# Optimization experiments

Measured on AMD Instinct MI355X. Metric: run time of the kernel, lower is better.

Reference implementation:

```python
import jax, jax.numpy as jnp
import numpy as np

EMBED_DIM = 768
NUM_HEADS = 12
HEAD_DIM = EMBED_DIM // NUM_HEADS


def setup_inputs() -> dict:
    key = jax.random.key(0)
    k_x, k_wqkv, k_bqkv, k_wp, k_bp = jax.random.split(key, 5)
    B, N, C = 4, 2048, EMBED_DIM
    # torch nn.Linear init scale ~ 1/sqrt(fan_in); use small normal for numerics
    s = 1.0 / np.sqrt(C)
    return {
        "x": jax.random.normal(k_x, (B, N, C), dtype=jnp.float32),
        "w_qkv": jax.random.normal(k_wqkv, (3 * C, C), dtype=jnp.float32) * s,  # torch [out,in]
        "b_qkv": jax.random.normal(k_bqkv, (3 * C,), dtype=jnp.float32) * s,
        "w_proj": jax.random.normal(k_wp, (C, C), dtype=jnp.float32) * s,
        "b_proj": jax.random.normal(k_bp, (C,), dtype=jnp.float32) * s,
    }


def reference(x, w_qkv, b_qkv, w_proj, b_proj):
    B, N, C = x.shape
    H, D = NUM_HEADS, HEAD_DIM
    scale = 1.0 / np.sqrt(D)
    # qkv linear: x @ W.T + b  -> [B,N,3C]
    qkv = jnp.einsum("bnc,oc->bno", x, w_qkv) + b_qkv
    qkv = qkv.reshape(B, N, 3, H, D).transpose(2, 0, 3, 1, 4)  # [3,B,H,N,D]
    q, k, v = qkv[0], qkv[1], qkv[2]
    attn = jnp.einsum("bhnd,bhmd->bhnm", q, k) * scale  # [B,H,N,N]
    attn = jax.nn.softmax(attn, axis=-1)
    out = jnp.einsum("bhnm,bhmd->bhnd", attn, v)  # [B,H,N,D]
    out = out.transpose(0, 2, 1, 3).reshape(B, N, C)
    return jnp.einsum("bnc,oc->bno", out, w_proj) + b_proj
```

## Files before the change

### kernel.cpp

```cpp
#include <hip/hip_runtime.h>
#include <hip/hip_bf16.h>
#include <math.h>

#define EMBED 768
#define NHEAD 12
#define HDIM 64
#define SEQ 2048
#define BATCH 4

typedef __hip_bfloat16 bf16;
typedef __attribute__((ext_vector_type(8))) short bf16x8;
typedef __attribute__((ext_vector_type(4))) short s16x4;
typedef __attribute__((ext_vector_type(4))) float f32x4;
typedef __attribute__((ext_vector_type(2))) unsigned int u32x2;

__device__ inline float b2f(bf16 v) { return __bfloat162float(v); }
__device__ inline bf16 f2b(float v) { return __float2bfloat16(v); }
__device__ inline unsigned pk2(float a, float b) {
  return (unsigned)__bfloat16_as_ushort(f2b(a)) |
         ((unsigned)__bfloat16_as_ushort(f2b(b)) << 16);
}

__device__ inline void gl_lds16(const bf16* g, bf16* l) {
  __builtin_amdgcn_global_load_lds(
      (const __attribute__((address_space(1))) void*)g,
      (__attribute__((address_space(3))) void*)l, 16, 0, 0);
}

#define NX4  (BATCH * SEQ * EMBED / 4)
#define NWQ4 (3 * EMBED * EMBED / 4)
#define NWP4 (EMBED * EMBED / 4)

__global__ __launch_bounds__(256) void cvt_all(
    const float* __restrict__ x, const float* __restrict__ wq,
    const float* __restrict__ wp, bf16* __restrict__ xb,
    bf16* __restrict__ wqb, bf16* __restrict__ wpb) {
  int i = blockIdx.x * 256 + threadIdx.x;
  const float* src;
  bf16* dst;
  int k;
  if (i < NX4) {
    src = x; dst = xb; k = i;
  } else if (i < NX4 + NWQ4) {
    src = wq; dst = wqb; k = i - NX4;
  } else if (i < NX4 + NWQ4 + NWP4) {
    src = wp; dst = wpb; k = i - NX4 - NWQ4;
  } else {
    return;
  }
  float4 v = ((const float4*)src)[k];
  s16x4 o;
  o[0] = (short)__bfloat16_as_ushort(f2b(v.x));
  o[1] = (short)__bfloat16_as_ushort(f2b(v.y));
  o[2] = (short)__bfloat16_as_ushort(f2b(v.z));
  o[3] = (short)__bfloat16_as_ushort(f2b(v.w));
  *(s16x4*)(dst + 4 * (size_t)k) = o;
}

template <int MODE, int TM>
__global__ __launch_bounds__(256, 4) void gemm_mfma(
    const bf16* __restrict__ A, const bf16* __restrict__ W,
    const float* __restrict__ bias, float* __restrict__ outF,
    bf16* __restrict__ outQ, bf16* __restrict__ outK, bf16* __restrict__ outV,
    int M, int N, int K) {
  __shared__ bf16 As[TM][64];
  __shared__ bf16 Bs[128][64];
  const int t = threadIdx.x;
  const int w = t >> 6;
  const int lane = t & 63;
  const int g = lane >> 4, c = lane & 15;
  const int m0 = blockIdx.y * TM, n0 = blockIdx.x * 128;
  constexpr int MJ = TM / 32;
  const int wr = (w >> 1) * (TM / 2);
  const int wc = (w & 1) * 64;

  const int srow = lane >> 3;
  const int l8 = lane & 7;
  const int sseg = (l8 ^ srow) * 8;

  f32x4 acc[4][MJ] = {};

  for (int k0 = 0; k0 < K; k0 += 64) {
#pragma unroll
    for (int i = 0; i < 4; i++) {
      int r = w * 32 + i * 8;
      gl_lds16(W + (size_t)(n0 + r + srow) * K + k0 + sseg, &Bs[r][0]);
    }
#pragma unroll
    for (int i = 0; i < TM / 32; i++) {
      int r = w * (TM / 4) + i * 8;
      gl_lds16(A + (size_t)(m0 + r + srow) * K + k0 + sseg, &As[r][0]);
    }
    __syncthreads();

#pragma unroll
    for (int h = 0; h < 2; h++) {
      bf16x8 xf[MJ], wf[4];
#pragma unroll
      for (int j = 0; j < MJ; j++)
        xf[j] = *(const bf16x8*)&As[wr + j * 16 + c][((h * 4 + g) ^ (c & 7)) * 8];
#pragma unroll
      for (int i = 0; i < 4; i++)
        wf[i] = *(const bf16x8*)&Bs[wc + i * 16 + c][((h * 4 + g) ^ (c & 7)) * 8];
#pragma unroll
      for (int i = 0; i < 4; i++)
#pragma unroll
        for (int j = 0; j < MJ; j++)
          acc[i][j] = __builtin_amdgcn_mfma_f32_16x16x32_bf16(wf[i], xf[j],
                                                              acc[i][j], 0, 0, 0);
    }
    __syncthreads();
  }

#pragma unroll
  for (int i = 0; i < 4; i++) {
    const int ob = n0 + wc + i * 16 + g * 4;
    const f32x4 bv = *(const f32x4*)&bias[ob];
    int which = 0, hh = 0, d0 = 0;
    if (MODE == 0) {
      which = ob / EMBED;
      int rem = ob - which * EMBED;
      hh = rem >> 6;
      d0 = rem & 63;
    }
#pragma unroll
    for (int j = 0; j < MJ; j++) {
      const int m = m0 + wr + j * 16 + c;
      f32x4 v = acc[i][j] + bv;
      if (MODE == 0) {
        const int bb = m >> 11, n = m & 2047;
        const size_t bh = (size_t)bb * NHEAD + hh;
        if (which == 0) {
          s16x4 q4;
#pragma unroll
          for (int r = 0; r < 4; r++)
            q4[r] = (short)__bfloat16_as_ushort(f2b(v[r] * 0.1803368801f));
          *(s16x4*)&outQ[(bh * SEQ + n) * HDIM + d0] = q4;
        } else if (which == 1) {
          s16x4 k4;
#pragma unroll
          for (int r = 0; r < 4; r++)
            k4[r] = (short)__bfloat16_as_ushort(f2b(v[r]));
          *(s16x4*)&outK[(bh * SEQ + n) * HDIM + d0] = k4;
        } else {
#pragma unroll
          for (int r = 0; r < 4; r++)
            outV[(bh * HDIM + d0 + r) * SEQ + n] = f2b(v[r]);
        }
      } else {
        *(f32x4*)&outF[(size_t)m * N + ob] = v;
      }
    }
  }
}

__global__ __launch_bounds__(256, 4) void attn_mfma(
    const bf16* __restrict__ Q, const bf16* __restrict__ Kk,
    const bf16* __restrict__ V, bf16* __restrict__ O) {
  __shared__ bf16 Ks[64 * 64];
  __shared__ bf16 Vts[64 * 64];
  __shared__ bf16 Pt[8][16 * 72];

  const int blk = blockIdx.x;
  const int bh = blk >> 4;
  const int qt = blk & 15;
  const int bb = bh / NHEAD;
  const int h = bh % NHEAD;
  const int t = threadIdx.x;
  const int lane = t & 63;
  const int w = t >> 6;
  const int g = lane >> 4;
  const int c = lane & 15;
  const size_t base = (size_t)bh * SEQ * HDIM;
  const int mb0 = qt * 128 + w * 16;
  const int mb1 = mb0 + 64;

  const int r8 = lane >> 3;
  const int l8 = lane & 7;
  const int gch = l8 ^ (r8 & 7);
  const int q0 = w * 2, q1 = w * 2 + 1;

  bf16x8 qa[2][2];
#pragma unroll
  for (int kh = 0; kh < 2; kh++) {
    qa[0][kh] = *(const bf16x8*)(Q + base + (size_t)(mb0 + c) * HDIM + kh * 32 + g * 8);
    qa[1][kh] = *(const bf16x8*)(Q + base + (size_t)(mb1 + c) * HDIM + kh * 32 + g * 8);
  }

  bf16x8 ones;
#pragma unroll
  for (int i = 0; i < 8; i++) ones[i] = (short)0x3F80;

  f32x4 o[2][4] = {};
  f32x4 o_l[2] = {};

  gl_lds16(Kk + base + (size_t)(q0 * 8 + r8) * HDIM + gch * 8, &Ks[q0 * 8 * 64]);
  gl_lds16(Kk + base + (size_t)(q1 * 8 + r8) * HDIM + gch * 8, &Ks[q1 * 8 * 64]);
  gl_lds16(V + base + (size_t)(q0 * 8 + r8) * SEQ + gch * 8, &Vts[q0 * 8 * 64]);
  gl_lds16(V + base + (size_t)(q1 * 8 + r8) * SEQ + gch * 8, &Vts[q1 * 8 * 64]);
  __syncthreads();

  bf16* const Pt0 = Pt[w * 2];
  bf16* const Pt1 = Pt[w * 2 + 1];

  for (int jt = 0; jt < SEQ / 64; jt++) {
    f32x4 s[2][4] = {};
#pragma unroll
    for (int nt = 0; nt < 4; nt++) {
#pragma unroll
      for (int kh = 0; kh < 2; kh++) {
        bf16x8 kb = *(const bf16x8*)&Ks[(nt * 16 + c) * 64 + ((kh * 4 + g) ^ (c & 7)) * 8];
        s[0][nt] = __builtin_amdgcn_mfma_f32_16x16x32_bf16(kb, qa[0][kh], s[0][nt], 0, 0, 0);
        s[1][nt] = __builtin_amdgcn_mfma_f32_16x16x32_bf16(kb, qa[1][kh], s[1][nt], 0, 0, 0);
      }
    }

    __syncthreads();
    if (jt + 1 < SEQ / 64) {
      const int jb = (jt + 1) * 64;
      gl_lds16(Kk + base + (size_t)(jb + q0 * 8 + r8) * HDIM + gch * 8, &Ks[q0 * 8 * 64]);
      gl_lds16(Kk + base + (size_t)(jb + q1 * 8 + r8) * HDIM + gch * 8, &Ks[q1 * 8 * 64]);
    }

#pragma unroll
    for (int nt = 0; nt < 4; nt++) {
      float a0 = __builtin_amdgcn_exp2f(s[0][nt][0]);
      float a1 = __builtin_amdgcn_exp2f(s[0][nt][1]);
      float a2 = __builtin_amdgcn_exp2f(s[0][nt][2]);
      float a3 = __builtin_amdgcn_exp2f(s[0][nt][3]);
      u32x2 pw0 = {pk2(a0, a1), pk2(a2, a3)};
      *(u32x2*)&Pt0[c * 72 + nt * 16 + g * 4] = pw0;
      float b0 = __builtin_amdgcn_exp2f(s[1][nt][0]);
      float b1 = __builtin_amdgcn_exp2f(s[1][nt][1]);
      float b2 = __builtin_amdgcn_exp2f(s[1][nt][2]);
      float b3 = __builtin_amdgcn_exp2f(s[1][nt][3]);
      u32x2 pw1 = {pk2(b0, b1), pk2(b2, b3)};
      *(u32x2*)&Pt1[c * 72 + nt * 16 + g * 4] = pw1;
    }
    bf16x8 pb[2][2];
    pb[0][0] = *(const bf16x8*)&Pt0[c * 72 + g * 8];
    pb[0][1] = *(const bf16x8*)&Pt0[c * 72 + 32 + g * 8];
    pb[1][0] = *(const bf16x8*)&Pt1[c * 72 + g * 8];
    pb[1][1] = *(const bf16x8*)&Pt1[c * 72 + 32 + g * 8];

#pragma unroll
    for (int dt = 0; dt < 4; dt++) {
      bf16x8 vb0 = *(const bf16x8*)&Vts[(dt * 16 + c) * 64 + ((0 + g) ^ (c & 7)) * 8];
      bf16x8 vb1 = *(const bf16x8*)&Vts[(dt * 16 + c) * 64 + ((4 + g) ^ (c & 7)) * 8];
      o[0][dt] = __builtin_amdgcn_mfma_f32_16x16x32_bf16(vb0, pb[0][0], o[0][dt], 0, 0, 0);
      o[0][dt] = __builtin_amdgcn_mfma_f32_16x16x32_bf16(vb1, pb[0][1], o[0][dt], 0, 0, 0);
      o[1][dt] = __builtin_amdgcn_mfma_f32_16x16x32_bf16(vb0, pb[1][0], o[1][dt], 0, 0, 0);
      o[1][dt] = __builtin_amdgcn_mfma_f32_16x16x32_bf16(vb1, pb[1][1], o[1][dt], 0, 0, 0);
    }
    o_l[0] = __builtin_amdgcn_mfma_f32_16x16x32_bf16(ones, pb[0][0], o_l[0], 0, 0, 0);
    o_l[0] = __builtin_amdgcn_mfma_f32_16x16x32_bf16(ones, pb[0][1], o_l[0], 0, 0, 0);
    o_l[1] = __builtin_amdgcn_mfma_f32_16x16x32_bf16(ones, pb[1][0], o_l[1], 0, 0, 0);
    o_l[1] = __builtin_amdgcn_mfma_f32_16x16x32_bf16(ones, pb[1][1], o_l[1], 0, 0, 0);

    __syncthreads();
    if (jt + 1 < SEQ / 64) {
      const int jb = (jt + 1) * 64;
      gl_lds16(V + base + (size_t)(q0 * 8 + r8) * SEQ + jb + gch * 8, &Vts[q0 * 8 * 64]);
      gl_lds16(V + base + (size_t)(q1 * 8 + r8) * SEQ + jb + gch * 8, &Vts[q1 * 8 * 64]);
    }
  }

#pragma unroll
  for (int grp = 0; grp < 2; grp++) {
    const float inv = __builtin_amdgcn_rcpf(o_l[grp][0]);
    const int mb = grp ? mb1 : mb0;
    const size_t rowoff = ((size_t)bb * SEQ + mb + c) * EMBED + h * 64 + g * 4;
#pragma unroll
    for (int dt = 0; dt < 4; dt++) {
      s16x4 ov;
#pragma unroll
      for (int r = 0; r < 4; r++)
        ov[r] = (short)__bfloat16_as_ushort(f2b(o[grp][dt][r] * inv));
      *(s16x4*)&O[rowoff + dt * 16] = ov;
    }
  }
}

extern "C" void kernel_launch(void* const* d_in, const int* in_sizes, int n_in,
                              void* d_out, int out_size, void* d_ws,
                              size_t ws_size, hipStream_t stream) {
  const float* x      = (const float*)d_in[0];
  const float* w_qkv  = (const float*)d_in[1];
  const float* b_qkv  = (const float*)d_in[2];
  const float* w_proj = (const float*)d_in[3];
  const float* b_proj = (const float*)d_in[4];

  const size_t per = (size_t)BATCH * NHEAD * SEQ * HDIM;
  bf16* Qp = (bf16*)d_ws;
  bf16* Kp = Qp + per;
  bf16* Vp = Kp + per;
  bf16* xb = Vp + per;
  bf16* wqkvb = xb + per;
  bf16* wprojb = wqkvb + (size_t)3 * EMBED * EMBED;
  bf16* AO = xb;

  const int ncvt = NX4 + NWQ4 + NWP4;
  cvt_all<<<dim3((ncvt + 255) / 256), 256, 0, stream>>>(x, w_qkv, w_proj, xb,
                                                        wqkvb, wprojb);

  dim3 g1(2304 / 128, 8192 / 128);
  gemm_mfma<0, 128><<<g1, 256, 0, stream>>>(xb, wqkvb, b_qkv, nullptr, Qp, Kp,
                                            Vp, BATCH * SEQ, 3 * EMBED, EMBED);

  attn_mfma<<<dim3(BATCH * NHEAD * (SEQ / 128)), 256, 0, stream>>>(Qp, Kp, Vp, AO);

  dim3 g2(768 / 128, 8192 / 64);
  gemm_mfma<1, 64><<<g2, 256, 0, stream>>>(AO, wprojb, b_proj, (float*)d_out,
                                           nullptr, nullptr, nullptr,
                                           BATCH * SEQ, EMBED, EMBED);
}
```

Measured before the change: 220.6 us.

## Use 256x256 double-buffered tile for QKV projection GEMM

Splits the QKV GEMM into a dedicated kernel with 512 threads, a 256x256 output tile and double-buffered LDS so the next K-slice loads asynchronously while MFMAs run on the current one. Larger tiles raise reuse of the A and W operands and cut global traffic. The cost is 128KB of LDS per block and a large accumulator footprint, which lowers occupancy. The grid shrinks to 288 blocks, which may underfill the CUs. The output projection GEMM is unchanged apart from dropping the mode template.

```diff
diff --git a/kernel.cpp b/kernel.cpp
--- a/kernel.cpp
+++ b/kernel.cpp
@@ -57,12 +57,105 @@
   *(s16x4*)(dst + 4 * (size_t)k) = o;
 }
 
-template <int MODE, int TM>
-__global__ __launch_bounds__(256, 4) void gemm_mfma(
+__global__ __launch_bounds__(512, 2) void gemm_qkv(
     const bf16* __restrict__ A, const bf16* __restrict__ W,
-    const float* __restrict__ bias, float* __restrict__ outF,
-    bf16* __restrict__ outQ, bf16* __restrict__ outK, bf16* __restrict__ outV,
-    int M, int N, int K) {
+    const float* __restrict__ bias, bf16* __restrict__ outQ,
+    bf16* __restrict__ outK, bf16* __restrict__ outV, int K) {
+  __shared__ bf16 As[2][256][64];
+  __shared__ bf16 Bs[2][256][64];
+  const int t = threadIdx.x;
+  const int w = t >> 6;
+  const int lane = t & 63;
+  const int g = lane >> 4, c = lane & 15;
+  const int m0 = blockIdx.y * 256, n0 = blockIdx.x * 256;
+  const int wr = (w >> 2) * 128;
+  const int wc = (w & 3) * 64;
+
+  const int srow = lane >> 3;
+  const int l8 = lane & 7;
+  const int sseg = (l8 ^ srow) * 8;
+
+  f32x4 acc[4][8] = {};
+  const int nsteps = K >> 6;
+
+#pragma unroll
+  for (int i = 0; i < 4; i++) {
+    int r = w * 32 + i * 8;
+    gl_lds16(A + (size_t)(m0 + r + srow) * K + sseg, &As[0][r][0]);
+    gl_lds16(W + (size_t)(n0 + r + srow) * K + sseg, &Bs[0][r][0]);
+  }
+  __syncthreads();
+
+  for (int s = 0; s < nsteps; s++) {
+    const int p = s & 1;
+    if (s + 1 < nsteps) {
+      const int k0 = (s + 1) << 6;
+#pragma unroll
+      for (int i = 0; i < 4; i++) {
+        int r = w * 32 + i * 8;
+        gl_lds16(A + (size_t)(m0 + r + srow) * K + k0 + sseg, &As[p ^ 1][r][0]);
+        gl_lds16(W + (size_t)(n0 + r + srow) * K + k0 + sseg, &Bs[p ^ 1][r][0]);
+      }
+    }
+
+#pragma unroll
+    for (int h = 0; h < 2; h++) {
+      bf16x8 xf[8], wf[4];
+#pragma unroll
+      for (int j = 0; j < 8; j++)
+        xf[j] = *(const bf16x8*)&As[p][wr + j * 16 + c][((h * 4 + g) ^ (c & 7)) * 8];
+#pragma unroll
+      for (int i = 0; i < 4; i++)
+        wf[i] = *(const bf16x8*)&Bs[p][wc + i * 16 + c][((h * 4 + g) ^ (c & 7)) * 8];
+#pragma unroll
+      for (int i = 0; i < 4; i++)
+#pragma unroll
+        for (int j = 0; j < 8; j++)
+          acc[i][j] = __builtin_amdgcn_mfma_f32_16x16x32_bf16(wf[i], xf[j],
+                                                              acc[i][j], 0, 0, 0);
+    }
+    __syncthreads();
+  }
+
+#pragma unroll
+  for (int i = 0; i < 4; i++) {
+    const int ob = n0 + wc + i * 16 + g * 4;
+    const f32x4 bv = *(const f32x4*)&bias[ob];
+    const int which = ob / EMBED;
+    const int rem = ob - which * EMBED;
+    const int hh = rem >> 6;
+    const int d0 = rem & 63;
+#pragma unroll
+    for (int j = 0; j < 8; j++) {
+      const int m = m0 + wr + j * 16 + c;
+      f32x4 v = acc[i][j] + bv;
+      const int bb = m >> 11, n = m & 2047;
+      const size_t bh = (size_t)bb * NHEAD + hh;
+      if (which == 0) {
+        s16x4 q4;
+#pragma unroll
+        for (int r = 0; r < 4; r++)
+          q4[r] = (short)__bfloat16_as_ushort(f2b(v[r] * 0.1803368801f));
+        *(s16x4*)&outQ[(bh * SEQ + n) * HDIM + d0] = q4;
+      } else if (which == 1) {
+        s16x4 k4;
+#pragma unroll
+        for (int r = 0; r < 4; r++)
+          k4[r] = (short)__bfloat16_as_ushort(f2b(v[r]));
+        *(s16x4*)&outK[(bh * SEQ + n) * HDIM + d0] = k4;
+      } else {
+#pragma unroll
+        for (int r = 0; r < 4; r++)
+          outV[(bh * HDIM + d0 + r) * SEQ + n] = f2b(v[r]);
+      }
+    }
+  }
+}
+
+template <int TM>
+__global__ __launch_bounds__(256, 4) void gemm_proj(
+    const bf16* __restrict__ A, const bf16* __restrict__ W,
+    const float* __restrict__ bias, float* __restrict__ outF, int N, int K) {
   __shared__ bf16 As[TM][64];
   __shared__ bf16 Bs[128][64];
   const int t = threadIdx.x;
@@ -116,40 +209,11 @@
   for (int i = 0; i < 4; i++) {
     const int ob = n0 + wc + i * 16 + g * 4;
     const f32x4 bv = *(const f32x4*)&bias[ob];
-    int which = 0, hh = 0, d0 = 0;
-    if (MODE == 0) {
-      which = ob / EMBED;
-      int rem = ob - which * EMBED;
-      hh = rem >> 6;
-      d0 = rem & 63;
-    }
 #pragma unroll
     for (int j = 0; j < MJ; j++) {
       const int m = m0 + wr + j * 16 + c;
       f32x4 v = acc[i][j] + bv;
-      if (MODE == 0) {
-        const int bb = m >> 11, n = m & 2047;
-        const size_t bh = (size_t)bb * NHEAD + hh;
-        if (which == 0) {
-          s16x4 q4;
-#pragma unroll
-          for (int r = 0; r < 4; r++)
-            q4[r] = (short)__bfloat16_as_ushort(f2b(v[r] * 0.1803368801f));
-          *(s16x4*)&outQ[(bh * SEQ + n) * HDIM + d0] = q4;
-        } else if (which == 1) {
-          s16x4 k4;
-#pragma unroll
-          for (int r = 0; r < 4; r++)
-            k4[r] = (short)__bfloat16_as_ushort(f2b(v[r]));
-          *(s16x4*)&outK[(bh * SEQ + n) * HDIM + d0] = k4;
-        } else {
-#pragma unroll
-          for (int r = 0; r < 4; r++)
-            outV[(bh * HDIM + d0 + r) * SEQ + n] = f2b(v[r]);
-        }
-      } else {
-        *(f32x4*)&outF[(size_t)m * N + ob] = v;
-      }
+      *(f32x4*)&outF[(size_t)m * N + ob] = v;
     }
   }
 }
@@ -303,14 +367,12 @@
   cvt_all<<<dim3((ncvt + 255) / 256), 256, 0, stream>>>(x, w_qkv, w_proj, xb,
                                                         wqkvb, wprojb);
 
-  dim3 g1(2304 / 128, 8192 / 128);
-  gemm_mfma<0, 128><<<g1, 256, 0, stream>>>(xb, wqkvb, b_qkv, nullptr, Qp, Kp,
-                                            Vp, BATCH * SEQ, 3 * EMBED, EMBED);
+  dim3 g1(2304 / 256, 8192 / 256);
+  gemm_qkv<<<g1, 512, 0, stream>>>(xb, wqkvb, b_qkv, Qp, Kp, Vp, EMBED);
 
   attn_mfma<<<dim3(BATCH * NHEAD * (SEQ / 128)), 256, 0, stream>>>(Qp, Kp, Vp, AO);
 
   dim3 g2(768 / 128, 8192 / 64);
-  gemm_mfma<1, 64><<<g2, 256, 0, stream>>>(AO, wprojb, b_proj, (float*)d_out,
-                                           nullptr, nullptr, nullptr,
-                                           BATCH * SEQ, EMBED, EMBED);
-}
+  gemm_proj<64><<<g2, 256, 0, stream>>>(AO, wprojb, b_proj, (float*)d_out,
+                                        EMBED, EMBED);
+}
```

After: 233.3 us. +5.7%, slower.
